# Kernel optimization log

Hardware: AMD Instinct MI355X
Metric: run time of the kernel (lower is better)

Reference implementation:

```python
import jax, jax.numpy as jnp
import numpy as np

DIM_IN = 1024
LAMBDA_SQ = float(DIM_IN)  # registered buffer: torch.tensor([float(dim_in)])
INIT_ETA = 0.001


def setup_inputs() -> dict:
    key = jax.random.key(0)
    k1, k2, k3, k4 = jax.random.split(key, 4)
    B, D = 128, DIM_IN
    W_t = jax.random.normal(k1, (B, D, D), dtype=jnp.float32)
    x_t = jax.random.normal(k2, (B, D), dtype=jnp.float32)
    grad_l_in = jax.random.normal(k3, (B, D), dtype=jnp.float32)
    # eta_proj: Linear(dim_in, 1); xavier-uniform weight, bias = init_eta
    bound = float(np.sqrt(6.0 / (D + 1)))
    eta_w = jax.random.uniform(k4, (1, D), minval=-bound, maxval=bound, dtype=jnp.float32)
    eta_b = jnp.full((1,), INIT_ETA, dtype=jnp.float32)
    return {"W_t": W_t, "x_t": x_t, "grad_l_in": grad_l_in, "eta_w": eta_w, "eta_b": eta_b}


def reference(W_t, x_t, grad_l_in, eta_w, eta_b):
    # eta_t = softplus(eta_proj(x_t)) -> [B, 1]
    eta_t = jax.nn.softplus(x_t @ eta_w.T + eta_b)          # [B, 1]
    scale = 1.0 / (LAMBDA_SQ + eta_t)                       # [B, 1]
    # grad_l_in is 2D -> delta-rule branch of sherman_morrison_step
    y_hat = jnp.einsum('boi,bi->bo', W_t, x_t)              # [B, D]
    error = y_hat - grad_l_in                               # [B, D]
    update = error[:, :, None] * x_t[:, None, :]            # rank-1 outer, [B, D, D]
    return W_t - scale[:, :, None] * update
```

## Files before the change

### kernel.cpp

```cpp
#include <hip/hip_runtime.h>
#include <math.h>


typedef float f4 __attribute__((ext_vector_type(4)));

constexpr int D = 1024;
constexpr float LAMBDA_SQ = 1024.0f;
constexpr int ROWS_PER_WAVE = 4;
constexpr int WAVES_PER_BLOCK = 4;
constexpr int ROWS_PER_BLOCK = ROWS_PER_WAVE * WAVES_PER_BLOCK;
constexpr int BLOCKS_PER_BATCH = D / ROWS_PER_BLOCK;

__global__ __launch_bounds__(256, 4) void update_kernel(const float* __restrict__ W,
                                                        const float* __restrict__ x,
                                                        const float* __restrict__ g,
                                                        const float* __restrict__ eta_w,
                                                        const float* __restrict__ eta_b,
                                                        float* __restrict__ out) {
    const int tid  = threadIdx.x;
    const int b    = blockIdx.x / BLOCKS_PER_BATCH;
    const int row0 = (blockIdx.x % BLOCKS_PER_BATCH) * ROWS_PER_BLOCK;
    const int wave = tid >> 6;
    const int lane = tid & 63;
    const int row  = row0 + wave * ROWS_PER_WAVE;

    const f4 gv = *(const f4*)(g + (size_t)b * D + row);
    const float eb = eta_b[0];

    const f4* __restrict__ xv = (const f4*)(x + (size_t)b * D);
    f4 xreg[4];
    #pragma unroll
    for (int c = 0; c < 4; ++c) xreg[c] = xv[c * 64 + lane];

    const f4* __restrict__ ev = (const f4*)eta_w;
    f4 ereg[4];
    #pragma unroll
    for (int c = 0; c < 4; ++c) ereg[c] = ev[c * 64 + lane];

    const size_t base = ((size_t)b * D + row) * D;
    const f4* __restrict__ wrow = (const f4*)(W + base);
    f4* __restrict__ orow = (f4*)(out + base);

    f4 wreg[ROWS_PER_WAVE][4];
    #pragma unroll
    for (int r = 0; r < ROWS_PER_WAVE; ++r) {
        #pragma unroll
        for (int c = 0; c < 4; ++c) {
            wreg[r][c] = __builtin_nontemporal_load(&wrow[(size_t)r * (D / 4) + c * 64 + lane]);
        }
    }

    float p = 0.0f;
    #pragma unroll
    for (int c = 0; c < 4; ++c) {
        p += ereg[c].x * xreg[c].x + ereg[c].y * xreg[c].y
           + ereg[c].z * xreg[c].z + ereg[c].w * xreg[c].w;
    }
    #pragma unroll
    for (int off = 32; off > 0; off >>= 1) p += __shfl_xor(p, off);
    const float z = p + eb;
    const float sp = fmaxf(z, 0.0f) + log1pf(expf(-fabsf(z)));
    const float s = 1.0f / (LAMBDA_SQ + sp);

    float dot[ROWS_PER_WAVE];
    #pragma unroll
    for (int r = 0; r < ROWS_PER_WAVE; ++r) {
        float d = 0.0f;
        #pragma unroll
        for (int c = 0; c < 4; ++c) {
            d += wreg[r][c].x * xreg[c].x + wreg[r][c].y * xreg[c].y
               + wreg[r][c].z * xreg[c].z + wreg[r][c].w * xreg[c].w;
        }
        dot[r] = d;
    }

    #pragma unroll
    for (int off = 32; off > 0; off >>= 1) {
        #pragma unroll
        for (int r = 0; r < ROWS_PER_WAVE; ++r) dot[r] += __shfl_xor(dot[r], off);
    }

    #pragma unroll
    for (int r = 0; r < ROWS_PER_WAVE; ++r) {
        const float f = s * (dot[r] - gv[r]);
        #pragma unroll
        for (int c = 0; c < 4; ++c) {
            f4 o;
            o.x = wreg[r][c].x - f * xreg[c].x;
            o.y = wreg[r][c].y - f * xreg[c].y;
            o.z = wreg[r][c].z - f * xreg[c].z;
            o.w = wreg[r][c].w - f * xreg[c].w;
            __builtin_nontemporal_store(o, &orow[(size_t)r * (D / 4) + c * 64 + lane]);
        }
    }
}

extern "C" void kernel_launch(void* const* d_in, const int* in_sizes, int n_in,
                              void* d_out, int out_size, void* d_ws, size_t ws_size,
                              hipStream_t stream) {
    const float* W     = (const float*)d_in[0];
    const float* x     = (const float*)d_in[1];
    const float* g     = (const float*)d_in[2];
    const float* eta_w = (const float*)d_in[3];
    const float* eta_b = (const float*)d_in[4];
    float* out = (float*)d_out;

    const int B = in_sizes[1] / D;
    update_kernel<<<B * BLOCKS_PER_BATCH, 256, 0, stream>>>(W, x, g, eta_w, eta_b, out);
}
```

Measured before the change: 826.4 us.

## Make blocks persistent per batch slice with double-buffered register prefetch of W rows

Each block now handles 128 rows of one batch matrix instead of 16, looping over 16 iterations of 8 rows. The next rows are prefetched into a second register buffer while the current buffer is reduced and written back. This spreads the per-block x/eta loads and softplus cost across more rows and keeps loads in flight while stores drain. The grid shrinks to 1024 blocks, which may reduce how much memory parallelism the GPU can extract on this streaming, bandwidth-bound kernel.

```diff
diff --git a/kernel.cpp b/kernel.cpp
--- a/kernel.cpp
+++ b/kernel.cpp
@@ -6,10 +6,12 @@
 
 constexpr int D = 1024;
 constexpr float LAMBDA_SQ = 1024.0f;
-constexpr int ROWS_PER_WAVE = 4;
-constexpr int WAVES_PER_BLOCK = 4;
-constexpr int ROWS_PER_BLOCK = ROWS_PER_WAVE * WAVES_PER_BLOCK;
-constexpr int BLOCKS_PER_BATCH = D / ROWS_PER_BLOCK;
+constexpr int WAVES = 4;
+constexpr int ROWS_PER_WAVE = 2;
+constexpr int ROWS_PER_ITER = WAVES * ROWS_PER_WAVE;
+constexpr int BLOCKS_PER_BATCH = 8;
+constexpr int ROWS_PER_BLOCK = D / BLOCKS_PER_BATCH;
+constexpr int NIT = ROWS_PER_BLOCK / ROWS_PER_ITER;
 
 __global__ __launch_bounds__(256, 4) void update_kernel(const float* __restrict__ W,
                                                         const float* __restrict__ x,
@@ -19,13 +21,14 @@
                                                         float* __restrict__ out) {
     const int tid  = threadIdx.x;
     const int b    = blockIdx.x / BLOCKS_PER_BATCH;
-    const int row0 = (blockIdx.x % BLOCKS_PER_BATCH) * ROWS_PER_BLOCK;
+    const int blk  = blockIdx.x % BLOCKS_PER_BATCH;
     const int wave = tid >> 6;
     const int lane = tid & 63;
-    const int row  = row0 + wave * ROWS_PER_WAVE;
+    const int span = blk * ROWS_PER_BLOCK;
 
-    const f4 gv = *(const f4*)(g + (size_t)b * D + row);
-    const float eb = eta_b[0];
+    const float* __restrict__ Wb = W   + (size_t)b * D * D;
+    float*       __restrict__ Ob = out + (size_t)b * D * D;
+    const float* __restrict__ gb = g   + (size_t)b * D;
 
     const f4* __restrict__ xv = (const f4*)(x + (size_t)b * D);
     f4 xreg[4];
@@ -36,19 +39,25 @@
     f4 ereg[4];
     #pragma unroll
     for (int c = 0; c < 4; ++c) ereg[c] = ev[c * 64 + lane];
+    const float eb = eta_b[0];
 
-    const size_t base = ((size_t)b * D + row) * D;
-    const f4* __restrict__ wrow = (const f4*)(W + base);
-    f4* __restrict__ orow = (f4*)(out + base);
+    f4 bufA[ROWS_PER_WAVE][4], bufB[ROWS_PER_WAVE][4];
+    float gA[ROWS_PER_WAVE], gB[ROWS_PER_WAVE];
 
-    f4 wreg[ROWS_PER_WAVE][4];
-    #pragma unroll
-    for (int r = 0; r < ROWS_PER_WAVE; ++r) {
+    auto prefetch = [&](f4 (&buf)[ROWS_PER_WAVE][4], float (&gv)[ROWS_PER_WAVE], int t) {
+        const int row = span + t * ROWS_PER_ITER + wave * ROWS_PER_WAVE;
+        const f4* __restrict__ src = (const f4*)(Wb + (size_t)row * D);
         #pragma unroll
-        for (int c = 0; c < 4; ++c) {
-            wreg[r][c] = __builtin_nontemporal_load(&wrow[(size_t)r * (D / 4) + c * 64 + lane]);
+        for (int r = 0; r < ROWS_PER_WAVE; ++r) {
+            #pragma unroll
+            for (int c = 0; c < 4; ++c)
+                buf[r][c] = __builtin_nontemporal_load(&src[r * (D / 4) + c * 64 + lane]);
         }
-    }
+        #pragma unroll
+        for (int r = 0; r < ROWS_PER_WAVE; ++r) gv[r] = gb[row + r];
+    };
+
+    prefetch(bufA, gA, 0);
 
     float p = 0.0f;
     #pragma unroll
@@ -62,36 +71,47 @@
     const float sp = fmaxf(z, 0.0f) + log1pf(expf(-fabsf(z)));
     const float s = 1.0f / (LAMBDA_SQ + sp);
 
-    float dot[ROWS_PER_WAVE];
-    #pragma unroll
-    for (int r = 0; r < ROWS_PER_WAVE; ++r) {
-        float d = 0.0f;
+    auto compute = [&](f4 (&buf)[ROWS_PER_WAVE][4], float (&gv)[ROWS_PER_WAVE], int t) {
+        const int row = span + t * ROWS_PER_ITER + wave * ROWS_PER_WAVE;
+        float dot[ROWS_PER_WAVE];
         #pragma unroll
-        for (int c = 0; c < 4; ++c) {
-            d += wreg[r][c].x * xreg[c].x + wreg[r][c].y * xreg[c].y
-               + wreg[r][c].z * xreg[c].z + wreg[r][c].w * xreg[c].w;
+        for (int r = 0; r < ROWS_PER_WAVE; ++r) {
+            float d = 0.0f;
+            #pragma unroll
+            for (int c = 0; c < 4; ++c) {
+                d += buf[r][c].x * xreg[c].x + buf[r][c].y * xreg[c].y
+                   + buf[r][c].z * xreg[c].z + buf[r][c].w * xreg[c].w;
+            }
+            dot[r] = d;
         }
-        dot[r] = d;
-    }
+        #pragma unroll
+        for (int off = 32; off > 0; off >>= 1) {
+            #pragma unroll
+            for (int r = 0; r < ROWS_PER_WAVE; ++r) dot[r] += __shfl_xor(dot[r], off);
+        }
+        f4* __restrict__ dst = (f4*)(Ob + (size_t)row * D);
+        #pragma unroll
+        for (int r = 0; r < ROWS_PER_WAVE; ++r) {
+            const float f = s * (dot[r] - gv[r]);
+            #pragma unroll
+            for (int c = 0; c < 4; ++c) {
+                f4 o;
+                o.x = buf[r][c].x - f * xreg[c].x;
+                o.y = buf[r][c].y - f * xreg[c].y;
+                o.z = buf[r][c].z - f * xreg[c].z;
+                o.w = buf[r][c].w - f * xreg[c].w;
+                __builtin_nontemporal_store(o, &dst[r * (D / 4) + c * 64 + lane]);
+            }
+        }
+    };
 
     #pragma unroll
-    for (int off = 32; off > 0; off >>= 1) {
-        #pragma unroll
-        for (int r = 0; r < ROWS_PER_WAVE; ++r) dot[r] += __shfl_xor(dot[r], off);
-    }
-
-    #pragma unroll
-    for (int r = 0; r < ROWS_PER_WAVE; ++r) {
-        const float f = s * (dot[r] - gv[r]);
-        #pragma unroll
-        for (int c = 0; c < 4; ++c) {
-            f4 o;
-            o.x = wreg[r][c].x - f * xreg[c].x;
-            o.y = wreg[r][c].y - f * xreg[c].y;
-            o.z = wreg[r][c].z - f * xreg[c].z;
-            o.w = wreg[r][c].w - f * xreg[c].w;
-            __builtin_nontemporal_store(o, &orow[(size_t)r * (D / 4) + c * 64 + lane]);
-        }
+    for (int it2 = 0; it2 < NIT / 2; ++it2) {
+        const int tA = 2 * it2, tB = 2 * it2 + 1;
+        prefetch(bufB, gB, tB);
+        compute(bufA, gA, tA);
+        if (tB + 1 < NIT) prefetch(bufA, gA, tB + 1);
+        compute(bufB, gB, tB);
     }
 }
 
```

After: 837.1 us. About the same (+1.3%).
